# Optimization experiments

Hardware: AMD Instinct MI355X
Metric: run time of the kernel (lower is better)

The kernel has to match this reference:

```python
import jax, jax.numpy as jnp
import numpy as np

B, Ci, H, W_ = 8, 64, 128, 128
C = 2 * Ci  # output channels of the 1x1 conv


def setup_inputs() -> dict:
    key = jax.random.key(0)
    kx, kw, kb = jax.random.split(key, 3)
    x = jax.random.normal(kx, (B, Ci, H, W_), dtype=jnp.float32)
    # Conv2d(Ci, 2*Ci, 1x1) parameters (kaiming-ish scale)
    Wc = jax.random.normal(kw, (C, Ci), dtype=jnp.float32) * (1.0 / np.float32(np.sqrt(Ci)))
    bc = jax.random.normal(kb, (C,), dtype=jnp.float32) * 0.01
    return {"x": x, "Wc": Wc, "bc": bc}


def _local_attention(y):
    # y: [B, C, H, W] conv output. 3x3 neighborhood self-attention, zero padding.
    b, c, h, w = y.shape
    yp = jnp.pad(y, ((0, 0), (0, 0), (1, 1), (1, 1)))
    # patches[:, :, k] = shifted neighborhood k (row-major 3x3, matching F.unfold order)
    patches = jnp.stack(
        [yp[:, :, di:di + h, dj:dj + w] for di in range(3) for dj in range(3)],
        axis=2,
    )  # [B, C, 9, H, W]
    mid = patches[:, :, 4]  # center pixel query, [B, C, H, W]
    scale = np.float32(1.0 / np.sqrt(c))
    scores = jnp.einsum("bcnhw,bchw->bnhw", patches, mid) * scale  # [B, 9, H, W]
    attn = jax.nn.softmax(scores, axis=1)
    out = jnp.einsum("bnhw,bcnhw->bchw", attn, patches)  # [B, C, H, W]
    return out


def reference(x, Wc, bc):
    # 1x1 conv == channel matmul
    y = jnp.einsum("bihw,oi->bohw", x, Wc) + bc[None, :, None, None]
    return _local_attention(y)
```

## Files before the change

### kernel.cpp

```cpp
#include <hip/hip_runtime.h>
#include <hip/hip_bf16.h>

typedef __attribute__((ext_vector_type(8))) short short8;
typedef __attribute__((ext_vector_type(4))) float floatx4;

#define XS_STRIDE 72
#define QBASE 26128

__device__ __forceinline__ ushort f2bf(float f) {
    union { __hip_bfloat16 h; ushort u; } cv;
    cv.h = __float2bfloat16(f);
    return cv.u;
}
__device__ __forceinline__ float bflo(unsigned int u) { return __uint_as_float(u << 16); }
__device__ __forceinline__ float bfhi(unsigned int u) { return __uint_as_float(u & 0xffff0000u); }

__device__ __forceinline__ float dot8(uint4 p, const float* cf) {
    return bflo(p.x)*cf[0] + bfhi(p.x)*cf[1] + bflo(p.y)*cf[2] + bfhi(p.y)*cf[3]
         + bflo(p.z)*cf[4] + bfhi(p.z)*cf[5] + bflo(p.w)*cf[6] + bfhi(p.w)*cf[7];
}
__device__ __forceinline__ void fma8(uint4 p, float a, float* o) {
    o[0] += a*bflo(p.x); o[1] += a*bfhi(p.x); o[2] += a*bflo(p.y); o[3] += a*bfhi(p.y);
    o[4] += a*bflo(p.z); o[5] += a*bfhi(p.z); o[6] += a*bflo(p.w); o[7] += a*bfhi(p.w);
}

__device__ __forceinline__ float gsum8(float v) {
    v += __int_as_float(__builtin_amdgcn_update_dpp(0, __float_as_int(v), 0xB1, 0xF, 0xF, false));
    v += __int_as_float(__builtin_amdgcn_update_dpp(0, __float_as_int(v), 0x4E, 0xF, 0xF, false));
    v += __shfl_xor(v, 4);
    return v;
}

__device__ __forceinline__ char* orow_base(char* smc, int oy, int ox) {
    return smc + (ox < 17 ? oy * 4352 + ox * 256
                          : QBASE + oy * 4352 + (ox - 17) * 256);
}
__device__ __forceinline__ int oswz(int ox) {
    return (ox & 7) ^ (((ox >> 3) & 3) << 1);
}

__global__ __launch_bounds__(256, 2)
void attn_conv_fused(const float* __restrict__ x, const float* __restrict__ Wc,
                     const float* __restrict__ bc, float* __restrict__ out) {
    __shared__ __align__(16) unsigned char smem[52240];
    ushort* xs = (ushort*)smem;
    char* smc = (char*)smem;

    const int tid = threadIdx.x;
    const int rid = ((blockIdx.x & 7) << 7) | (blockIdx.x >> 3);
    const int b   = rid >> 7;
    const int h0  = ((rid >> 2) & 31) * 4;
    const int w0  = (rid & 3) * 32;
    const int lane = tid & 63;
    const int wv   = tid >> 6;

    if (tid < 204) {
        int py  = (tid * 965) >> 15;
        int pxx = tid - py * 34;
        int gh = h0 + py - 1, gw = w0 + pxx - 1;
        bool inb = (gh >= 0 && gh < 128 && gw >= 0 && gw < 128);
        ushort* dst = xs + tid * XS_STRIDE;
        if (inb) {
            const float* xp = x + (b * 64) * 16384 + gh * 128 + gw;
            #pragma unroll
            for (int c0 = 0; c0 < 64; c0 += 4) {
                float v0 = xp[(c0 + 0) << 14];
                float v1 = xp[(c0 + 1) << 14];
                float v2 = xp[(c0 + 2) << 14];
                float v3 = xp[(c0 + 3) << 14];
                unsigned int u01 = (unsigned int)f2bf(v0) | ((unsigned int)f2bf(v1) << 16);
                unsigned int u23 = (unsigned int)f2bf(v2) | ((unsigned int)f2bf(v3) << 16);
                *(uint2*)(dst + c0) = make_uint2(u01, u23);
            }
        } else {
            #pragma unroll
            for (int c0 = 0; c0 < 64; c0 += 4)
                *(uint2*)(dst + c0) = make_uint2(0u, 0u);
        }
    }

    const int col = lane & 15;
    const int kq  = lane >> 4;
    short8 bw[8][2];
    float  bias[8];
    #pragma unroll
    for (int t = 0; t < 8; ++t) {
        int c = t * 16 + col;
        bias[t] = bc[c];
        #pragma unroll
        for (int half = 0; half < 2; ++half) {
            const float* wp = Wc + c * 64 + half * 32 + kq * 8;
            float4 wa = *(const float4*)wp;
            float4 wb = *(const float4*)(wp + 4);
            short8 f;
            f[0] = (short)f2bf(wa.x); f[1] = (short)f2bf(wa.y);
            f[2] = (short)f2bf(wa.z); f[3] = (short)f2bf(wa.w);
            f[4] = (short)f2bf(wb.x); f[5] = (short)f2bf(wb.y);
            f[6] = (short)f2bf(wb.z); f[7] = (short)f2bf(wb.w);
            bw[t][half] = f;
        }
    }
    __syncthreads();

    short8 af0[4], af1[4];
    #pragma unroll
    for (int i = 0; i < 4; ++i) {
        int mt = wv + i * 4;
        if (mt < 13) {
            const ushort* ap = xs + (mt * 16 + col) * XS_STRIDE + kq * 8;
            af0[i] = *(const short8*)(ap);
            af1[i] = *(const short8*)(ap + 32);
        }
    }
    __syncthreads();

    char* wbase = smc + (col < 8 ? 0 : QBASE);
    const int cb2 = (col & 7) * 2;
    #pragma unroll
    for (int i = 0; i < 4; ++i) {
        int mt = wv + i * 4;
        if (mt < 13) {
            floatx4 acc[8];
            #pragma unroll
            for (int t = 0; t < 8; ++t) acc[t] = (floatx4){0.f, 0.f, 0.f, 0.f};
            #pragma unroll
            for (int t = 0; t < 8; ++t) {
                acc[t] = __builtin_amdgcn_mfma_f32_16x16x32_bf16(af0[i], bw[t][0], acc[t], 0, 0, 0);
                acc[t] = __builtin_amdgcn_mfma_f32_16x16x32_bf16(af1[i], bw[t][1], acc[t], 0, 0, 0);
            }
            #pragma unroll
            for (int r = 0; r < 4; ++r) {
                int pxr = mt * 16 + kq * 4 + r;
                if (pxr < 204) {
                    int py  = (pxr * 965) >> 15;
                    int pxx = pxr - py * 34;
                    int gh = h0 + py - 1, gw = w0 + pxx - 1;
                    bool inb = (gh >= 0 && gh < 128 && gw >= 0 && gw < 128);
                    char* prow = wbase + pxr * 128;
                    int swz = (pxr & 7) << 4;
                    #pragma unroll
                    for (int t = 0; t < 8; ++t)
                        *(ushort*)(prow + (((t * 16) ^ swz) + cb2)) =
                            f2bf(inb ? (acc[t][r] + bias[t]) : 0.f);
                }
            }
        }
    }
    __syncthreads();

    const int g  = tid & 7;
    const int ox = tid >> 3;
    const int osw = oswz(ox);
    for (int oy = 0; oy < 4; ++oy) {
        int pc = (oy + 1) * 34 + (ox + 1);
        uint4 plo[9], phi[9];
        #pragma unroll
        for (int n = 0; n < 9; ++n) {
            int pi = pc + (n / 3 - 1) * 34 + (n % 3 - 1);
            const char* pp = smc + pi * 128 + ((g * 16) ^ ((pi & 7) << 4));
            plo[n] = *(const uint4*)pp;
            phi[n] = *(const uint4*)(pp + QBASE);
        }
        float cf[16];
        {
            uint4 c0 = plo[4], c1 = phi[4];
            cf[0]=bflo(c0.x); cf[1]=bfhi(c0.x); cf[2]=bflo(c0.y); cf[3]=bfhi(c0.y);
            cf[4]=bflo(c0.z); cf[5]=bfhi(c0.z); cf[6]=bflo(c0.w); cf[7]=bfhi(c0.w);
            cf[8]=bflo(c1.x); cf[9]=bfhi(c1.x); cf[10]=bflo(c1.y); cf[11]=bfhi(c1.y);
            cf[12]=bflo(c1.z); cf[13]=bfhi(c1.z); cf[14]=bflo(c1.w); cf[15]=bfhi(c1.w);
        }
        float s[9];
        #pragma unroll
        for (int n = 0; n < 9; ++n)
            s[n] = dot8(plo[n], cf) + dot8(phi[n], cf + 8);
        #pragma unroll
        for (int n = 0; n < 9; ++n)
            s[n] = gsum8(s[n]) * 0.08838834764831845f;
        float m = s[0];
        #pragma unroll
        for (int n = 1; n < 9; ++n) m = fmaxf(m, s[n]);
        float e[9], sum = 0.f;
        #pragma unroll
        for (int n = 0; n < 9; ++n) { e[n] = __expf(s[n] - m); sum += e[n]; }
        float inv = 1.f / sum;

        float o[16];
        #pragma unroll
        for (int j = 0; j < 16; ++j) o[j] = 0.f;
        #pragma unroll
        for (int n = 0; n < 9; ++n) {
            float a = e[n] * inv;
            fma8(plo[n], a, o);
            fma8(phi[n], a, o + 8);
        }

        #pragma unroll
        for (int H = 0; H < 2; ++H) {
            __syncthreads();
            if ((g >> 2) == H) {
                char* rb = orow_base(smc, oy, ox);
                int gg = g & 3;
                #pragma unroll
                for (int k = 0; k < 4; ++k)
                    *(float4*)(rb + (((gg * 4 + k) ^ osw) << 4)) =
                        make_float4(o[4*k], o[4*k+1], o[4*k+2], o[4*k+3]);
            }
            __syncthreads();
            {
                int cl = tid >> 2, q = tid & 3;
                int c  = H * 64 + cl;
                float tmp[8];
                #pragma unroll
                for (int j = 0; j < 8; ++j) {
                    int oxr = (j < 4) ? (q * 4 + j) : (16 + q * 4 + (j - 4));
                    const char* rb = orow_base(smc, oy, oxr);
                    tmp[j] = *(const float*)(rb + (((cl >> 2) ^ oswz(oxr)) << 4) + ((cl & 3) << 2));
                }
                float* og = out + ((size_t)((b * 128 + c) * 128 + (h0 + oy))) * 128 + w0;
                *(float4*)(og + q * 4)      = make_float4(tmp[0], tmp[1], tmp[2], tmp[3]);
                *(float4*)(og + 16 + q * 4) = make_float4(tmp[4], tmp[5], tmp[6], tmp[7]);
            }
        }
    }
}

extern "C" void kernel_launch(void* const* d_in, const int* in_sizes, int n_in,
                              void* d_out, int out_size, void* d_ws, size_t ws_size,
                              hipStream_t stream) {
    const float* x  = (const float*)d_in[0];
    const float* Wc = (const float*)d_in[1];
    const float* bc = (const float*)d_in[2];
    float* out = (float*)d_out;

    dim3 grid(1024);
    dim3 block(256);
    attn_conv_fused<<<grid, block, 0, stream>>>(x, Wc, bc, out);
}
```

Before: 128.4 us.

## Reuse neighbor rows via rolling window and store outputs directly without LDS transpose

The attention phase now keeps a rolling 3-row window of neighborhood patches in registers, so each new output row loads only one new patch row from LDS instead of all nine neighbors. It uses packed float2 arithmetic for the score and weighted-sum accumulation, and applies the softmax normalization once at the end. The LDS transpose and its two barriers per half-row are removed; each thread writes its 16 channels straight to global memory with scalar stores strided by a channel plane. This cuts LDS traffic and synchronization but makes global stores less coalesced (32 consecutive floats per channel row across the ox lanes) and raises register pressure.

Result: no change. 127.4 us (-0.7%).

```diff
diff --git a/kernel.cpp b/kernel.cpp
--- a/kernel.cpp
+++ b/kernel.cpp
@@ -3,6 +3,7 @@
 
 typedef __attribute__((ext_vector_type(8))) short short8;
 typedef __attribute__((ext_vector_type(4))) float floatx4;
+typedef __attribute__((ext_vector_type(2))) float floatx2;
 
 #define XS_STRIDE 72
 #define QBASE 26128
@@ -14,14 +15,12 @@
 }
 __device__ __forceinline__ float bflo(unsigned int u) { return __uint_as_float(u << 16); }
 __device__ __forceinline__ float bfhi(unsigned int u) { return __uint_as_float(u & 0xffff0000u); }
-
-__device__ __forceinline__ float dot8(uint4 p, const float* cf) {
-    return bflo(p.x)*cf[0] + bfhi(p.x)*cf[1] + bflo(p.y)*cf[2] + bfhi(p.y)*cf[3]
-         + bflo(p.z)*cf[4] + bfhi(p.z)*cf[5] + bflo(p.w)*cf[6] + bfhi(p.w)*cf[7];
-}
-__device__ __forceinline__ void fma8(uint4 p, float a, float* o) {
-    o[0] += a*bflo(p.x); o[1] += a*bfhi(p.x); o[2] += a*bflo(p.y); o[3] += a*bfhi(p.y);
-    o[4] += a*bflo(p.z); o[5] += a*bfhi(p.z); o[6] += a*bflo(p.w); o[7] += a*bfhi(p.w);
+__device__ __forceinline__ floatx2 bf2f2(unsigned int u) {
+    floatx2 r; r.x = __uint_as_float(u << 16); r.y = __uint_as_float(u & 0xffff0000u); return r;
+}
+__device__ __forceinline__ void fmaacc(uint4 p, floatx2 a2, floatx2* o2) {
+    o2[0] += a2 * bf2f2(p.x); o2[1] += a2 * bf2f2(p.y);
+    o2[2] += a2 * bf2f2(p.z); o2[3] += a2 * bf2f2(p.w);
 }
 
 __device__ __forceinline__ float gsum8(float v) {
@@ -31,13 +30,76 @@
     return v;
 }
 
-__device__ __forceinline__ char* orow_base(char* smc, int oy, int ox) {
-    return smc + (ox < 17 ? oy * 4352 + ox * 256
-                          : QBASE + oy * 4352 + (ox - 17) * 256);
-}
-__device__ __forceinline__ int oswz(int ox) {
-    return (ox & 7) ^ (((ox >> 3) & 3) << 1);
-}
+#define LOADROW(S, PROW)                                                            \
+    {                                                                               \
+        _Pragma("unroll")                                                           \
+        for (int dx = 0; dx < 3; ++dx) {                                            \
+            int pi = (PROW) * 34 + ox + dx;                                         \
+            const char* pp = smc + pi * 128 + ((g * 16) ^ ((pi & 7) << 4));         \
+            wlo[S][dx] = *(const uint4*)pp;                                         \
+            whi[S][dx] = *(const uint4*)(pp + QBASE);                               \
+        }                                                                           \
+    }
+
+#define SCORE1(S, DX) ({                                                            \
+        uint4 _l = wlo[S][DX], _h = whi[S][DX];                                     \
+        floatx2 _s = bf2f2(_l.x) * cf2[0];                                          \
+        _s += bf2f2(_l.y) * cf2[1];                                                 \
+        _s += bf2f2(_l.z) * cf2[2];                                                 \
+        _s += bf2f2(_l.w) * cf2[3];                                                 \
+        _s += bf2f2(_h.x) * cf2[4];                                                 \
+        _s += bf2f2(_h.y) * cf2[5];                                                 \
+        _s += bf2f2(_h.z) * cf2[6];                                                 \
+        _s += bf2f2(_h.w) * cf2[7];                                                 \
+        _s.x + _s.y; })
+
+#define PV(S, DX, A)                                                                \
+    {                                                                               \
+        floatx2 _a2; _a2.x = (A); _a2.y = (A);                                      \
+        fmaacc(wlo[S][DX], _a2, o2);                                                \
+        fmaacc(whi[S][DX], _a2, o2 + 4);                                            \
+    }
+
+#define ATTN_OY(OY, ST, SM, SB)                                                     \
+    {                                                                               \
+        floatx2 cf2[8];                                                             \
+        {                                                                           \
+            uint4 c0 = wlo[SM][1], c1 = whi[SM][1];                                 \
+            cf2[0] = bf2f2(c0.x); cf2[1] = bf2f2(c0.y);                             \
+            cf2[2] = bf2f2(c0.z); cf2[3] = bf2f2(c0.w);                             \
+            cf2[4] = bf2f2(c1.x); cf2[5] = bf2f2(c1.y);                             \
+            cf2[6] = bf2f2(c1.z); cf2[7] = bf2f2(c1.w);                             \
+        }                                                                           \
+        float s[9];                                                                 \
+        s[0] = SCORE1(ST, 0); s[1] = SCORE1(ST, 1); s[2] = SCORE1(ST, 2);           \
+        s[3] = SCORE1(SM, 0); s[4] = SCORE1(SM, 1); s[5] = SCORE1(SM, 2);           \
+        s[6] = SCORE1(SB, 0); s[7] = SCORE1(SB, 1); s[8] = SCORE1(SB, 2);           \
+        _Pragma("unroll")                                                           \
+        for (int n = 0; n < 9; ++n)                                                 \
+            s[n] = gsum8(s[n]) * 0.08838834764831845f;             \
+        float m = s[0];                                                             \
+        _Pragma("unroll")                                                           \
+        for (int n = 1; n < 9; ++n) m = fmaxf(m, s[n]);                             \
+        float e[9], sum = 0.f;                                                      \
+        _Pragma("unroll")                                                           \
+        for (int n = 0; n < 9; ++n) { e[n] = __expf(s[n] - m); sum += e[n]; }       \
+        floatx2 o2[8];                                                              \
+        _Pragma("unroll")                                                           \
+        for (int k = 0; k < 8; ++k) { o2[k].x = 0.f; o2[k].y = 0.f; }               \
+        PV(ST, 0, e[0]) PV(ST, 1, e[1]) PV(ST, 2, e[2])                             \
+        PV(SM, 0, e[3]) PV(SM, 1, e[4]) PV(SM, 2, e[5])                             \
+        PV(SB, 0, e[6]) PV(SB, 1, e[7]) PV(SB, 2, e[8])                             \
+        float inv = 1.f / sum;                                                      \
+        floatx2 inv2; inv2.x = inv; inv2.y = inv;                                   \
+        float* og = out + ((size_t)((b * 128 + g * 16) * 128 + (h0 + (OY)))) * 128  \
+                    + w0 + ox;                                                      \
+        _Pragma("unroll")                                                           \
+        for (int k = 0; k < 8; ++k) {                                               \
+            floatx2 v = o2[k] * inv2;                                               \
+            og[(2 * k) * 16384]     = v.x;                                          \
+            og[(2 * k + 1) * 16384] = v.y;                                          \
+        }                                                                           \
+    }
 
 __global__ __launch_bounds__(256, 2)
 void attn_conv_fused(const float* __restrict__ x, const float* __restrict__ Wc,
@@ -150,78 +212,16 @@
 
     const int g  = tid & 7;
     const int ox = tid >> 3;
-    const int osw = oswz(ox);
-    for (int oy = 0; oy < 4; ++oy) {
-        int pc = (oy + 1) * 34 + (ox + 1);
-        uint4 plo[9], phi[9];
-        #pragma unroll
-        for (int n = 0; n < 9; ++n) {
-            int pi = pc + (n / 3 - 1) * 34 + (n % 3 - 1);
-            const char* pp = smc + pi * 128 + ((g * 16) ^ ((pi & 7) << 4));
-            plo[n] = *(const uint4*)pp;
-            phi[n] = *(const uint4*)(pp + QBASE);
-        }
-        float cf[16];
-        {
-            uint4 c0 = plo[4], c1 = phi[4];
-            cf[0]=bflo(c0.x); cf[1]=bfhi(c0.x); cf[2]=bflo(c0.y); cf[3]=bfhi(c0.y);
-            cf[4]=bflo(c0.z); cf[5]=bfhi(c0.z); cf[6]=bflo(c0.w); cf[7]=bfhi(c0.w);
-            cf[8]=bflo(c1.x); cf[9]=bfhi(c1.x); cf[10]=bflo(c1.y); cf[11]=bfhi(c1.y);
-            cf[12]=bflo(c1.z); cf[13]=bfhi(c1.z); cf[14]=bflo(c1.w); cf[15]=bfhi(c1.w);
-        }
-        float s[9];
-        #pragma unroll
-        for (int n = 0; n < 9; ++n)
-            s[n] = dot8(plo[n], cf) + dot8(phi[n], cf + 8);
-        #pragma unroll
-        for (int n = 0; n < 9; ++n)
-            s[n] = gsum8(s[n]) * 0.08838834764831845f;
-        float m = s[0];
-        #pragma unroll
-        for (int n = 1; n < 9; ++n) m = fmaxf(m, s[n]);
-        float e[9], sum = 0.f;
-        #pragma unroll
-        for (int n = 0; n < 9; ++n) { e[n] = __expf(s[n] - m); sum += e[n]; }
-        float inv = 1.f / sum;
-
-        float o[16];
-        #pragma unroll
-        for (int j = 0; j < 16; ++j) o[j] = 0.f;
-        #pragma unroll
-        for (int n = 0; n < 9; ++n) {
-            float a = e[n] * inv;
-            fma8(plo[n], a, o);
-            fma8(phi[n], a, o + 8);
-        }
-
-        #pragma unroll
-        for (int H = 0; H < 2; ++H) {
-            __syncthreads();
-            if ((g >> 2) == H) {
-                char* rb = orow_base(smc, oy, ox);
-                int gg = g & 3;
-                #pragma unroll
-                for (int k = 0; k < 4; ++k)
-                    *(float4*)(rb + (((gg * 4 + k) ^ osw) << 4)) =
-                        make_float4(o[4*k], o[4*k+1], o[4*k+2], o[4*k+3]);
-            }
-            __syncthreads();
-            {
-                int cl = tid >> 2, q = tid & 3;
-                int c  = H * 64 + cl;
-                float tmp[8];
-                #pragma unroll
-                for (int j = 0; j < 8; ++j) {
-                    int oxr = (j < 4) ? (q * 4 + j) : (16 + q * 4 + (j - 4));
-                    const char* rb = orow_base(smc, oy, oxr);
-                    tmp[j] = *(const float*)(rb + (((cl >> 2) ^ oswz(oxr)) << 4) + ((cl & 3) << 2));
-                }
-                float* og = out + ((size_t)((b * 128 + c) * 128 + (h0 + oy))) * 128 + w0;
-                *(float4*)(og + q * 4)      = make_float4(tmp[0], tmp[1], tmp[2], tmp[3]);
-                *(float4*)(og + 16 + q * 4) = make_float4(tmp[4], tmp[5], tmp[6], tmp[7]);
-            }
-        }
-    }
+    uint4 wlo[3][3], whi[3][3];
+
+    LOADROW(0, 0) LOADROW(1, 1) LOADROW(2, 2)
+    ATTN_OY(0, 0, 1, 2)
+    LOADROW(0, 3)
+    ATTN_OY(1, 1, 2, 0)
+    LOADROW(1, 4)
+    ATTN_OY(2, 2, 0, 1)
+    LOADROW(2, 5)
+    ATTN_OY(3, 0, 1, 2)
 }
 
 extern "C" void kernel_launch(void* const* d_in, const int* in_sizes, int n_in,
```
